# Optimization experiments

Measured on AMD Instinct MI355X. Metric: run time of the kernel, lower is better.

The kernel has to match this reference:

```python
import jax, jax.numpy as jnp
import numpy as np

NUM_HEADS = 16
NEG_INF = -1e9  # matches torch source's -1000000000.0 additive mask
ROPE_BASE = 10000.0


def _rope(t):
    """Rotary position embedding, half-rotation form. t: [B, H, S, D]."""
    D = t.shape[-1]
    S = t.shape[2]
    inv_freq = 1.0 / (ROPE_BASE ** (jnp.arange(0, D, 2, dtype=jnp.float32) / D))  # [D/2]
    pos = jnp.arange(S, dtype=jnp.float32)
    freqs = pos[:, None] * inv_freq[None, :]          # [S, D/2]
    cos = jnp.cos(freqs)[None, None]                  # [1,1,S,D/2]
    sin = jnp.sin(freqs)[None, None]
    t1, t2 = t[..., : D // 2], t[..., D // 2 :]
    return jnp.concatenate([t1 * cos - t2 * sin, t1 * sin + t2 * cos], axis=-1)


def setup_inputs() -> dict:
    key = jax.random.key(0)
    kx, kq, kk, kv, ko = jax.random.split(key, 5)
    B, S, Dm = 2, 2048, 1024
    w_scale = 0.02
    return {
        "x": jax.random.normal(kx, (B, S, Dm), dtype=jnp.float32),
        "attention_mask": jnp.ones((B, S), dtype=jnp.float32),
        "Wq": jax.random.normal(kq, (Dm, Dm), dtype=jnp.float32) * w_scale,
        "Wk": jax.random.normal(kk, (Dm, Dm), dtype=jnp.float32) * w_scale,
        "Wv": jax.random.normal(kv, (Dm, Dm), dtype=jnp.float32) * w_scale,
        "Wo": jax.random.normal(ko, (Dm, Dm), dtype=jnp.float32) * w_scale,
    }


def reference(x, attention_mask, Wq, Wk, Wv, Wo):
    B, S, Dm = x.shape
    H = NUM_HEADS
    Hd = Dm // H

    def to_heads(t):  # [B,S,Dm] -> [B,H,S,Hd]
        return t.reshape(B, S, H, Hd).transpose(0, 2, 1, 3)

    q = _rope(to_heads(x @ Wq))
    k = _rope(to_heads(x @ Wk))
    v = to_heads(x @ Wv)

    scaling = 1.0 / np.sqrt(Hd).astype(np.float32)
    scores = jnp.einsum("bhqd,bhkd->bhqk", q, k) * scaling  # [B,H,S,S]

    # causal additive mask (triu of -1e9 above diagonal), as in apply_masking
    causal = jnp.triu(jnp.full((S, S), NEG_INF, dtype=scores.dtype), k=1)
    # padding mask: (1 - mask) * -1e9 broadcast to [B,1,1,S]
    amask = (1.0 - attention_mask)[:, None, None, :] * NEG_INF
    scores = scores + causal[None, None] + amask

    weights = jax.nn.softmax(scores, axis=-1)
    out = jnp.einsum("bhqk,bhkd->bhqd", weights, v)  # [B,H,S,Hd]
    out = out.transpose(0, 2, 1, 3).reshape(B, S, Dm)
    return out @ Wo
```

## Files before the change

### kernel.cpp

```cpp
#include <hip/hip_runtime.h>

typedef unsigned short u16;
typedef unsigned int u32;
typedef __attribute__((ext_vector_type(8))) short short8;
typedef __attribute__((ext_vector_type(4))) short s4v;
typedef __attribute__((ext_vector_type(4))) float f32x4;

#define S_LEN 2048
#define NH 16
#define HD 64
#define DM 1024

#if __has_builtin(__builtin_amdgcn_mfma_f32_16x16x16_bf16)
#define MFMA_K16(a, b, c) __builtin_amdgcn_mfma_f32_16x16x16_bf16(a, b, c, 0, 0, 0)
#else
#define MFMA_K16(a, b, c) __builtin_amdgcn_mfma_f32_16x16x16bf16_1k(a, b, c, 0, 0, 0)
#endif

__device__ __forceinline__ u16 f2bf(float f) {
    union { float f; u32 u; } v; v.f = f;
    u32 u = v.u;
    u32 r = u + 0x7fffu + ((u >> 16) & 1u);
    return (u16)(r >> 16);
}
__device__ __forceinline__ float bf2f(u16 h) {
    union { u32 u; float f; } v; v.u = ((u32)h) << 16;
    return v.f;
}

__device__ __forceinline__ u32 cvtpk_bf16(float lo, float hi) {
    u32 r;
    asm("v_cvt_pk_bf16_f32 %0, %1, %2" : "=v"(r) : "v"(lo), "v"(hi));
    return r;
}

__device__ __forceinline__ void load_lds16(const u16* g, u16* l) {
    __builtin_amdgcn_global_load_lds((const __attribute__((address_space(1))) void*)g,
                                     (__attribute__((address_space(3))) void*)l, 16, 0, 0);
}

__global__ __launch_bounds__(256) void cvt_bf16(const float* __restrict__ in, u16* __restrict__ out, int n) {
    int i = (blockIdx.x * 256 + threadIdx.x) * 4;
    if (i < n) {
        float4 v = *(const float4*)(in + i);
        ushort4 o;
        o.x = f2bf(v.x); o.y = f2bf(v.y); o.z = f2bf(v.z); o.w = f2bf(v.w);
        *(ushort4*)(out + i) = o;
    }
}

__global__ __launch_bounds__(256) void transpose_w4(const float* __restrict__ W0, const float* __restrict__ W1,
                                                    const float* __restrict__ W2, const float* __restrict__ W3,
                                                    u16* __restrict__ T0, u16* __restrict__ T1,
                                                    u16* __restrict__ T2, u16* __restrict__ T3) {
    __shared__ float tile[32][33];
    int z = blockIdx.z;
    const float* W = (z == 0) ? W0 : (z == 1) ? W1 : (z == 2) ? W2 : W3;
    u16* Wt = (z == 0) ? T0 : (z == 1) ? T1 : (z == 2) ? T2 : T3;
    int tx = threadIdx.x, ty = threadIdx.y;
    int k0 = blockIdx.y * 32, n0 = blockIdx.x * 32;
    #pragma unroll
    for (int j = 0; j < 32; j += 8)
        tile[ty + j][tx] = W[(size_t)(k0 + ty + j) * DM + n0 + tx];
    __syncthreads();
    #pragma unroll
    for (int j = 0; j < 32; j += 8)
        Wt[(size_t)(n0 + ty + j) * DM + k0 + tx] = f2bf(tile[tx][ty + j]);
}

template<int MODE, int NI>
__global__ __launch_bounds__(256) void gemm128(const u16* __restrict__ A, const u16* __restrict__ Bt,
                                               u16* __restrict__ Qh, u16* __restrict__ Kh,
                                               u16* __restrict__ Vh, float* __restrict__ Cf) {
    __shared__ u16 Al[128 * 64];
    __shared__ u16 Bl[NI * 32 * 64];
    const int K = DM;
    int tid = threadIdx.x;
    int wave = tid >> 6, lane = tid & 63, g = lane >> 4, ln = lane & 15;
    int wm = (wave >> 1) * 64, wn = (wave & 1) * (NI * 16);
    size_t mb0 = (size_t)blockIdx.y * 128, nb0 = (size_t)blockIdx.x * (NI * 32);

    f32x4 acc[4][NI];
    #pragma unroll
    for (int i = 0; i < 4; i++)
        #pragma unroll
        for (int j = 0; j < NI; j++)
            acc[i][j] = (f32x4){0.f, 0.f, 0.f, 0.f};

    int srow = lane >> 3;
    int scol = (lane & 7) ^ srow;
    const u16* Ag = A + (mb0 + wave * 32 + srow) * K + scol * 8;
    u16* Alw = Al + wave * 2048;
    const u16* Bg;
    u16* Blw;
    if (NI == 4) {
        Bg = Bt + (nb0 + wave * 32 + srow) * K + scol * 8;
        Blw = Bl + wave * 2048;
    } else {
        Bg = Bt + (nb0 + wave * 16 + srow) * K + scol * 8;
        Blw = Bl + wave * 1024;
    }
    int cswz = ln & 7;

    for (int k0 = 0; k0 < K; k0 += 64) {
        __syncthreads();
        #pragma unroll
        for (int c = 0; c < 4; c++)
            load_lds16(Ag + (size_t)(c * 8) * K + k0, Alw + c * 512);
        #pragma unroll
        for (int c = 0; c < (NI == 4 ? 4 : 2); c++)
            load_lds16(Bg + (size_t)(c * 8) * K + k0, Blw + c * 512);
        __syncthreads();
        short8 af[2][4], bf[2][NI];
        #pragma unroll
        for (int ks = 0; ks < 2; ks++) {
            #pragma unroll
            for (int i = 0; i < 4; i++)
                af[ks][i] = *(const short8*)&Al[(wm + i * 16 + ln) * 64 + (((ks * 4 + g) ^ cswz) * 8)];
            #pragma unroll
            for (int i = 0; i < NI; i++)
                bf[ks][i] = *(const short8*)&Bl[(wn + i * 16 + ln) * 64 + (((ks * 4 + g) ^ cswz) * 8)];
        }
        #pragma unroll
        for (int ks = 0; ks < 2; ks++)
            #pragma unroll
            for (int mi = 0; mi < 4; mi++)
                #pragma unroll
                for (int ni = 0; ni < NI; ni++)
                    acc[mi][ni] = __builtin_amdgcn_mfma_f32_16x16x32_bf16(af[ks][mi], bf[ks][ni], acc[mi][ni], 0, 0, 0);
    }

    if (MODE == 1) {
        #pragma unroll
        for (int mi = 0; mi < 4; mi++)
            #pragma unroll
            for (int ni = 0; ni < NI; ni++)
                #pragma unroll
                for (int r = 0; r < 4; r++) {
                    int m = (int)mb0 + wm + mi * 16 + g * 4 + r;
                    int n = (int)nb0 + wn + ni * 16 + ln;
                    Cf[(size_t)m * DM + n] = acc[mi][ni][r];
                }
    } else {
        int nbase = (int)nb0 + wn;
        int which = nbase >> 10;
        int h = (nbase & (DM - 1)) >> 6;
        if (which < 2) {
            u16* dst = (which == 0) ? Qh : Kh;
            float inv0 = exp2f(-0.4152408746976557f * (float)ln);
            float inv1 = exp2f(-0.4152408746976557f * (float)(16 + ln));
            #pragma unroll
            for (int mi = 0; mi < 4; mi++) {
                #pragma unroll
                for (int r = 0; r < 4; r++) {
                    int m = (int)mb0 + wm + mi * 16 + g * 4 + r;
                    int b = m >> 11, s = m & (S_LEN - 1);
                    float fs = (float)s;
                    float sn0, cs0, sn1, cs1;
                    __sincosf(fs * inv0, &sn0, &cs0);
                    __sincosf(fs * inv1, &sn1, &cs1);
                    float a0 = acc[mi][0][r], a1 = acc[mi][1][r];
                    float a2 = acc[mi][2][r], a3 = acc[mi][3][r];
                    size_t base = ((size_t)(b * NH + h) * S_LEN + s) * HD;
                    dst[base + ln]      = f2bf(a0 * cs0 - a2 * sn0);
                    dst[base + 16 + ln] = f2bf(a1 * cs1 - a3 * sn1);
                    dst[base + 32 + ln] = f2bf(a0 * sn0 + a2 * cs0);
                    dst[base + 48 + ln] = f2bf(a1 * sn1 + a3 * cs1);
                }
            }
        } else {
            #pragma unroll
            for (int mi = 0; mi < 4; mi++) {
                #pragma unroll
                for (int r = 0; r < 4; r++) {
                    int m = (int)mb0 + wm + mi * 16 + g * 4 + r;
                    int b = m >> 11, s = m & (S_LEN - 1);
                    size_t base = ((size_t)(b * NH + h) * S_LEN + s) * HD;
                    #pragma unroll
                    for (int ni = 0; ni < 4; ni++)
                        Vh[base + ni * 16 + ln] = f2bf(acc[mi][ni][r]);
                }
            }
        }
    }
}

__global__ __launch_bounds__(256) void vtrans(const u16* __restrict__ Vh, u16* __restrict__ Vt) {
    __shared__ u16 t[64][70];
    int tid = threadIdx.x;
    int s0 = blockIdx.x * 64, bh = blockIdx.y;
    int r = tid >> 2, c = (tid & 3) * 8;
    const u16* src = Vh + ((size_t)bh * S_LEN + s0) * HD;
    *(short8*)&t[r][c]      = *(const short8*)(src + (size_t)r * HD + c);
    *(short8*)&t[r][c + 32] = *(const short8*)(src + (size_t)r * HD + c + 32);
    __syncthreads();
    u16* dst = Vt + ((size_t)bh * HD + r) * S_LEN + s0;
    short8 o0, o1;
    #pragma unroll
    for (int j = 0; j < 8; j++) {
        o0[j] = (short)t[c + j][r];
        o1[j] = (short)t[c + 32 + j][r];
    }
    *(short8*)(dst + c)      = o0;
    *(short8*)(dst + c + 32) = o1;
}

__global__ __launch_bounds__(512, 4) void flash_kernel(const u16* __restrict__ Qh, const u16* __restrict__ Kh,
                                                       const u16* __restrict__ Vt, const float* __restrict__ amask,
                                                       u16* __restrict__ Op0, u16* __restrict__ Op1,
                                                       u16* __restrict__ Op2, u16* __restrict__ Op3,
                                                       float* __restrict__ L0, float* __restrict__ L1,
                                                       float* __restrict__ L2, float* __restrict__ L3) {
    __shared__ u16 Kl[2][64 * 64];
    __shared__ u16 Vl[2][64 * 64];
    __shared__ float Ml[2][64];
    int tid = threadIdx.x;
    int wave = tid >> 6, lane = tid & 63, g = lane >> 4, ln = lane & 15;
    int qblk = 15 - ((int)blockIdx.x >> 2);
    int sp = blockIdx.x & 3;
    int bh = blockIdx.y;
    int b = bh >> 4;
    int q0 = qblk * 128 + wave * 16;
    int qv = q0 + ln;
    const u16* Qb = Qh + (size_t)bh * (S_LEN * HD);
    const u16* Kb = Kh + (size_t)bh * (S_LEN * HD);
    const u16* Vb = Vt + (size_t)bh * (S_LEN * HD);
    const float* am = amask + b * S_LEN;

    short8 qa0 = *(const short8*)(Qb + (size_t)(q0 + ln) * HD + g * 8);
    short8 qa1 = *(const short8*)(Qb + (size_t)(q0 + ln) * HD + 32 + g * 8);

    f32x4 O[4];
    #pragma unroll
    for (int i = 0; i < 4; i++) O[i] = (f32x4){0.f, 0.f, 0.f, 0.f};
    float lsum = 0.f;
    const float SCL = 0.125f * 1.4426950408889634f;
    const float MSCL = -1.4426950408889634e9f;

    int T = 2 * qblk + 2;
    int srow = tid >> 3, scid = tid & 7, s7 = srow & 7;
    int stoff = srow * 64 + ((scid ^ s7) * 8);
    const u16* KgL = Kb + (size_t)srow * HD + ((scid ^ s7) * 8);
    const u16* VgP = Vb + (size_t)srow * S_LEN + scid * 8;
    bool vswap = (wave & 1);

    int l7 = ln & 7;
    int kc0 = (g ^ l7) * 8;
    int kc1 = ((4 + g) ^ l7) * 8;
    int rbq = ln * 64;
    int vcoff[4];
    #pragma unroll
    for (int n0 = 0; n0 < 4; n0++)
        vcoff[n0] = (((n0 * 2 + (g >> 1)) ^ l7) * 8) + ((((g & 1) ^ (ln >> 3)) & 1) * 4);

    load_lds16(KgL + (size_t)(sp * 64) * HD, &Kl[0][wave * 512]);
    short8 vR = *(const short8*)(VgP + sp * 64);
    float mR = 0.f;
    if (tid < 64) mR = (1.0f - am[sp * 64 + tid]) * MSCL;
    int cur = 0;

    for (int kt = sp; kt < T; kt += 4) {
        int kbase = kt * 64;
        short8 vS = vR;
        if (vswap) vS = __builtin_shufflevector(vR, vR, 4, 5, 6, 7, 0, 1, 2, 3);
        *(short8*)(Vl[cur] + stoff) = vS;
        if (tid < 64) Ml[cur][tid] = mR;
        __syncthreads();

        if (kt + 4 < T) {
            load_lds16(KgL + (size_t)(kbase + 256) * HD, &Kl[cur ^ 1][wave * 512]);
            vR = *(const short8*)(VgP + (kbase + 256));
            if (tid < 64) mR = (1.0f - am[kbase + 256 + tid]) * MSCL;
        }

        if (kbase <= q0 + 15) {
            const u16* Klc = Kl[cur];
            const u16* Vlc = Vl[cur];
            u32 pk[4][2];
            bool needmask = (kbase + 63 > q0);

            if (!needmask) {
                #pragma unroll
                for (int n0 = 0; n0 < 4; n0++) {
                    const u16* kr = Klc + (n0 * 16) * 64 + rbq;
                    short8 kb0 = *(const short8*)(kr + kc0);
                    short8 kb1 = *(const short8*)(kr + kc1);
                    f32x4 sv = (f32x4){0.f, 0.f, 0.f, 0.f};
                    sv = __builtin_amdgcn_mfma_f32_16x16x32_bf16(kb0, qa0, sv, 0, 0, 0);
                    sv = __builtin_amdgcn_mfma_f32_16x16x32_bf16(kb1, qa1, sv, 0, 0, 0);
                    f32x4 mkv = *(f32x4*)&Ml[cur][n0 * 16 + g * 4];
                    float p[4];
                    #pragma unroll
                    for (int r = 0; r < 4; r++) {
                        p[r] = exp2f(sv[r] * SCL + mkv[r]);
                        lsum += p[r];
                    }
                    pk[n0][0] = cvtpk_bf16(p[0], p[1]);
                    pk[n0][1] = cvtpk_bf16(p[2], p[3]);
                }
            } else {
                #pragma unroll
                for (int n0 = 0; n0 < 4; n0++) {
                    const u16* kr = Klc + (n0 * 16) * 64 + rbq;
                    short8 kb0 = *(const short8*)(kr + kc0);
                    short8 kb1 = *(const short8*)(kr + kc1);
                    f32x4 sv = (f32x4){0.f, 0.f, 0.f, 0.f};
                    sv = __builtin_amdgcn_mfma_f32_16x16x32_bf16(kb0, qa0, sv, 0, 0, 0);
                    sv = __builtin_amdgcn_mfma_f32_16x16x32_bf16(kb1, qa1, sv, 0, 0, 0);
                    f32x4 mkv = *(f32x4*)&Ml[cur][n0 * 16 + g * 4];
                    int keyb = kbase + n0 * 16 + g * 4;
                    float p[4];
                    #pragma unroll
                    for (int r = 0; r < 4; r++) {
                        float s2 = sv[r] * SCL + mkv[r];
                        if (keyb + r > qv) s2 = -1.0e9f;
                        p[r] = exp2f(s2);
                        lsum += p[r];
                    }
                    pk[n0][0] = cvtpk_bf16(p[0], p[1]);
                    pk[n0][1] = cvtpk_bf16(p[2], p[3]);
                }
            }

            __builtin_amdgcn_s_setprio(1);
            #pragma unroll
            for (int t = 0; t < 4; t++) {
                const u16* vr = Vlc + (t * 16) * 64 + rbq;
                #pragma unroll
                for (int n0 = 0; n0 < 4; n0++) {
                    s4v va = *(const s4v*)(vr + vcoff[n0]);
                    union { u32 u[2]; s4v v; } pb;
                    pb.u[0] = pk[n0][0];
                    pb.u[1] = pk[n0][1];
                    O[t] = MFMA_K16(va, pb.v, O[t]);
                }
            }
            __builtin_amdgcn_s_setprio(0);
        }
        cur ^= 1;
    }

    lsum += __shfl_xor(lsum, 16, 64);
    lsum += __shfl_xor(lsum, 32, 64);
    u16* Od = (sp == 0) ? Op0 : (sp == 1) ? Op1 : (sp == 2) ? Op2 : Op3;
    float* Ld = (sp == 0) ? L0 : (sp == 1) ? L1 : (sp == 2) ? L2 : L3;
    if (lane < 16) Ld[(size_t)bh * S_LEN + q0 + ln] = lsum;
    size_t obase = (size_t)bh * (HD * S_LEN) + q0 + ln;
    #pragma unroll
    for (int t = 0; t < 4; t++)
        #pragma unroll
        for (int r = 0; r < 4; r++)
            Od[obase + (size_t)(t * 16 + g * 4 + r) * S_LEN] = f2bf(O[t][r]);
}

__global__ __launch_bounds__(256) void flash_reduce(const u16* __restrict__ Op0, const u16* __restrict__ Op1,
                                                    const u16* __restrict__ Op2, const u16* __restrict__ Op3,
                                                    const float* __restrict__ L0, const float* __restrict__ L1,
                                                    const float* __restrict__ L2, const float* __restrict__ L3,
                                                    u16* __restrict__ attn) {
    __shared__ float t[64][65];
    int tid = threadIdx.x;
    int qt = blockIdx.x, bh = blockIdx.y;
    int b = bh >> 4, h = bh & (NH - 1);
    #pragma unroll
    for (int it = 0; it < 2; it++) {
        int idx = tid + it * 256;
        int d = idx >> 3, c = (idx & 7) * 8;
        size_t off = (size_t)bh * (HD * S_LEN) + (size_t)d * S_LEN + qt * 64 + c;
        short8 a0 = *(const short8*)(Op0 + off);
        short8 a1 = *(const short8*)(Op1 + off);
        short8 a2 = *(const short8*)(Op2 + off);
        short8 a3 = *(const short8*)(Op3 + off);
        #pragma unroll
        for (int j = 0; j < 8; j++)
            t[d][c + j] = bf2f((u16)a0[j]) + bf2f((u16)a1[j]) + bf2f((u16)a2[j]) + bf2f((u16)a3[j]);
    }
    __syncthreads();
    int qr = tid >> 2, dc = (tid & 3) * 16;
    int qg = qt * 64 + qr;
    size_t li = (size_t)bh * S_LEN + qg;
    float inv = 1.0f / (L0[li] + L1[li] + L2[li] + L3[li]);
    short8 o0, o1;
    #pragma unroll
    for (int j = 0; j < 8; j++) {
        o0[j] = (short)f2bf(t[dc + j][qr] * inv);
        o1[j] = (short)f2bf(t[dc + 8 + j][qr] * inv);
    }
    u16* dst = attn + ((size_t)b * S_LEN + qg) * DM + h * HD + dc;
    *(short8*)dst = o0;
    *(short8*)(dst + 8) = o1;
}

extern "C" void kernel_launch(void* const* d_in, const int* in_sizes, int n_in,
                              void* d_out, int out_size, void* d_ws, size_t ws_size,
                              hipStream_t stream) {
    const float* x     = (const float*)d_in[0];
    const float* amask = (const float*)d_in[1];
    const float* Wq    = (const float*)d_in[2];
    const float* Wk    = (const float*)d_in[3];
    const float* Wv    = (const float*)d_in[4];
    const float* Wo    = (const float*)d_in[5];
    float* out = (float*)d_out;
    char* ws = (char*)d_ws;

    u16* x_bf   = (u16*)(ws);
    u16* Op1    = (u16*)(ws);
    u16* Wqkv_t = (u16*)(ws + 8388608);
    float* L0   = (float*)(ws + 8388608);
    float* L1   = (float*)(ws + 8650752);
    float* L2   = (float*)(ws + 8912896);
    float* L3   = (float*)(ws + 9175040);
    u16* Wo_t   = (u16*)(ws + 14680064);
    u16* Qh     = (u16*)(ws + 16777216);
    u16* Kh     = (u16*)(ws + 25165824);
    u16* Vt     = (u16*)(ws + 33554432);
    u16* attnF  = (u16*)(ws + 33554432);
    u16* Vh     = (u16*)(ws + 41943040);
    u16* Op0    = (u16*)(ws + 41943040);
    u16* Op2    = (u16*)d_out;
    u16* Op3    = (u16*)d_out + 4194304;

    cvt_bf16<<<4096, 256, 0, stream>>>(x, x_bf, 2 * S_LEN * DM);

    transpose_w4<<<dim3(32, 32, 4), dim3(32, 8), 0, stream>>>(
        Wq, Wk, Wv, Wo, Wqkv_t, Wqkv_t + 1048576, Wqkv_t + 2097152, Wo_t);

    gemm128<0, 4><<<dim3(24, 32), 256, 0, stream>>>(x_bf, Wqkv_t, Qh, Kh, Vh, nullptr);

    vtrans<<<dim3(32, 2 * NH), 256, 0, stream>>>(Vh, Vt);

    flash_kernel<<<dim3(64, 2 * NH), 512, 0, stream>>>(Qh, Kh, Vt, amask,
                                                       Op0, Op1, Op2, Op3, L0, L1, L2, L3);

    flash_reduce<<<dim3(32, 2 * NH), 256, 0, stream>>>(Op0, Op1, Op2, Op3,
                                                       L0, L1, L2, L3, attnF);

    gemm128<1, 2><<<dim3(16, 32), 256, 0, stream>>>(attnF, Wo_t, nullptr, nullptr, nullptr, out);
}
```

Baseline: 208.2 us.

## Load V tiles via direct-to-LDS async copy and precompute mask into registers

The vtrans kernel now writes V pre-swizzled, with the half-swap applied for odd row groups, and precomputes the scaled additive padding mask into a workspace buffer. The flash kernel then streams V tiles into LDS with the same direct global-to-LDS path used for K, and loads the mask straight into registers, removing the register-staged V store and the shared mask array. It also splits the row-sum accumulator into four independent lanes to shorten the dependency chain. This relies on the swizzle in vtrans matching the read offsets in flash and on the new workspace region not overlapping live buffers.

```diff
diff --git a/kernel.cpp b/kernel.cpp
--- a/kernel.cpp
+++ b/kernel.cpp
@@ -10,6 +10,7 @@
 #define NH 16
 #define HD 64
 #define DM 1024
+#define MSCL_C (-1.4426950408889634e9f)
 
 #if __has_builtin(__builtin_amdgcn_mfma_f32_16x16x16_bf16)
 #define MFMA_K16(a, b, c) __builtin_amdgcn_mfma_f32_16x16x16_bf16(a, b, c, 0, 0, 0)
@@ -185,10 +186,15 @@
     }
 }
 
-__global__ __launch_bounds__(256) void vtrans(const u16* __restrict__ Vh, u16* __restrict__ Vt) {
+__global__ __launch_bounds__(256) void vtrans(const u16* __restrict__ Vh, u16* __restrict__ Vt,
+                                              const float* __restrict__ amask, float* __restrict__ Mg) {
     __shared__ u16 t[64][70];
     int tid = threadIdx.x;
     int s0 = blockIdx.x * 64, bh = blockIdx.y;
+    if (bh == 0) {
+        int idx = blockIdx.x * 256 + tid;
+        if (idx < 2 * S_LEN) Mg[idx] = (1.0f - amask[idx]) * MSCL_C;
+    }
     int r = tid >> 2, c = (tid & 3) * 8;
     const u16* src = Vh + ((size_t)bh * S_LEN + s0) * HD;
     *(short8*)&t[r][c]      = *(const short8*)(src + (size_t)r * HD + c);
@@ -201,19 +207,22 @@
         o0[j] = (short)t[c + j][r];
         o1[j] = (short)t[c + 32 + j][r];
     }
+    if (r & 8) {
+        o0 = __builtin_shufflevector(o0, o0, 4, 5, 6, 7, 0, 1, 2, 3);
+        o1 = __builtin_shufflevector(o1, o1, 4, 5, 6, 7, 0, 1, 2, 3);
+    }
     *(short8*)(dst + c)      = o0;
     *(short8*)(dst + c + 32) = o1;
 }
 
 __global__ __launch_bounds__(512, 4) void flash_kernel(const u16* __restrict__ Qh, const u16* __restrict__ Kh,
-                                                       const u16* __restrict__ Vt, const float* __restrict__ amask,
+                                                       const u16* __restrict__ Vt, const float* __restrict__ Mg,
                                                        u16* __restrict__ Op0, u16* __restrict__ Op1,
                                                        u16* __restrict__ Op2, u16* __restrict__ Op3,
                                                        float* __restrict__ L0, float* __restrict__ L1,
                                                        float* __restrict__ L2, float* __restrict__ L3) {
     __shared__ u16 Kl[2][64 * 64];
     __shared__ u16 Vl[2][64 * 64];
-    __shared__ float Ml[2][64];
     int tid = threadIdx.x;
     int wave = tid >> 6, lane = tid & 63, g = lane >> 4, ln = lane & 15;
     int qblk = 15 - ((int)blockIdx.x >> 2);
@@ -225,7 +234,7 @@
     const u16* Qb = Qh + (size_t)bh * (S_LEN * HD);
     const u16* Kb = Kh + (size_t)bh * (S_LEN * HD);
     const u16* Vb = Vt + (size_t)bh * (S_LEN * HD);
-    const float* am = amask + b * S_LEN;
+    const float* Mb = Mg + b * S_LEN;
 
     short8 qa0 = *(const short8*)(Qb + (size_t)(q0 + ln) * HD + g * 8);
     short8 qa1 = *(const short8*)(Qb + (size_t)(q0 + ln) * HD + 32 + g * 8);
@@ -233,16 +242,13 @@
     f32x4 O[4];
     #pragma unroll
     for (int i = 0; i < 4; i++) O[i] = (f32x4){0.f, 0.f, 0.f, 0.f};
-    float lsum = 0.f;
+    f32x4 ls = (f32x4){0.f, 0.f, 0.f, 0.f};
     const float SCL = 0.125f * 1.4426950408889634f;
-    const float MSCL = -1.4426950408889634e9f;
 
     int T = 2 * qblk + 2;
     int srow = tid >> 3, scid = tid & 7, s7 = srow & 7;
-    int stoff = srow * 64 + ((scid ^ s7) * 8);
     const u16* KgL = Kb + (size_t)srow * HD + ((scid ^ s7) * 8);
-    const u16* VgP = Vb + (size_t)srow * S_LEN + scid * 8;
-    bool vswap = (wave & 1);
+    const u16* VgL = Vb + (size_t)srow * S_LEN + ((scid ^ s7) * 8);
 
     int l7 = ln & 7;
     int kc0 = (g ^ l7) * 8;
@@ -254,23 +260,27 @@
         vcoff[n0] = (((n0 * 2 + (g >> 1)) ^ l7) * 8) + ((((g & 1) ^ (ln >> 3)) & 1) * 4);
 
     load_lds16(KgL + (size_t)(sp * 64) * HD, &Kl[0][wave * 512]);
-    short8 vR = *(const short8*)(VgP + sp * 64);
-    float mR = 0.f;
-    if (tid < 64) mR = (1.0f - am[sp * 64 + tid]) * MSCL;
+    load_lds16(VgL + sp * 64, &Vl[0][wave * 512]);
+    f32x4 mkR[4];
+    #pragma unroll
+    for (int n0 = 0; n0 < 4; n0++)
+        mkR[n0] = *(const f32x4*)(Mb + sp * 64 + n0 * 16 + g * 4);
     int cur = 0;
 
     for (int kt = sp; kt < T; kt += 4) {
         int kbase = kt * 64;
-        short8 vS = vR;
-        if (vswap) vS = __builtin_shufflevector(vR, vR, 4, 5, 6, 7, 0, 1, 2, 3);
-        *(short8*)(Vl[cur] + stoff) = vS;
-        if (tid < 64) Ml[cur][tid] = mR;
         __syncthreads();
+
+        f32x4 mk[4];
+        #pragma unroll
+        for (int n0 = 0; n0 < 4; n0++) mk[n0] = mkR[n0];
 
         if (kt + 4 < T) {
             load_lds16(KgL + (size_t)(kbase + 256) * HD, &Kl[cur ^ 1][wave * 512]);
-            vR = *(const short8*)(VgP + (kbase + 256));
-            if (tid < 64) mR = (1.0f - am[kbase + 256 + tid]) * MSCL;
+            load_lds16(VgL + (kbase + 256), &Vl[cur ^ 1][wave * 512]);
+            #pragma unroll
+            for (int n0 = 0; n0 < 4; n0++)
+                mkR[n0] = *(const f32x4*)(Mb + kbase + 256 + n0 * 16 + g * 4);
         }
 
         if (kbase <= q0 + 15) {
@@ -288,12 +298,11 @@
                     f32x4 sv = (f32x4){0.f, 0.f, 0.f, 0.f};
                     sv = __builtin_amdgcn_mfma_f32_16x16x32_bf16(kb0, qa0, sv, 0, 0, 0);
                     sv = __builtin_amdgcn_mfma_f32_16x16x32_bf16(kb1, qa1, sv, 0, 0, 0);
-                    f32x4 mkv = *(f32x4*)&Ml[cur][n0 * 16 + g * 4];
                     float p[4];
                     #pragma unroll
                     for (int r = 0; r < 4; r++) {
-                        p[r] = exp2f(sv[r] * SCL + mkv[r]);
-                        lsum += p[r];
+                        p[r] = exp2f(sv[r] * SCL + mk[n0][r]);
+                        ls[r] += p[r];
                     }
                     pk[n0][0] = cvtpk_bf16(p[0], p[1]);
                     pk[n0][1] = cvtpk_bf16(p[2], p[3]);
@@ -307,15 +316,14 @@
                     f32x4 sv = (f32x4){0.f, 0.f, 0.f, 0.f};
                     sv = __builtin_amdgcn_mfma_f32_16x16x32_bf16(kb0, qa0, sv, 0, 0, 0);
                     sv = __builtin_amdgcn_mfma_f32_16x16x32_bf16(kb1, qa1, sv, 0, 0, 0);
-                    f32x4 mkv = *(f32x4*)&Ml[cur][n0 * 16 + g * 4];
                     int keyb = kbase + n0 * 16 + g * 4;
                     float p[4];
                     #pragma unroll
                     for (int r = 0; r < 4; r++) {
-                        float s2 = sv[r] * SCL + mkv[r];
+                        float s2 = sv[r] * SCL + mk[n0][r];
                         if (keyb + r > qv) s2 = -1.0e9f;
                         p[r] = exp2f(s2);
-                        lsum += p[r];
+                        ls[r] += p[r];
                     }
                     pk[n0][0] = cvtpk_bf16(p[0], p[1]);
                     pk[n0][1] = cvtpk_bf16(p[2], p[3]);
@@ -340,6 +348,7 @@
         cur ^= 1;
     }
 
+    float lsum = (ls[0] + ls[1]) + (ls[2] + ls[3]);
     lsum += __shfl_xor(lsum, 16, 64);
     lsum += __shfl_xor(lsum, 32, 64);
     u16* Od = (sp == 0) ? Op0 : (sp == 1) ? Op1 : (sp == 2) ? Op2 : Op3;
@@ -410,6 +419,7 @@
     float* L1   = (float*)(ws + 8650752);
     float* L2   = (float*)(ws + 8912896);
     float* L3   = (float*)(ws + 9175040);
+    float* Mg   = (float*)(ws + 9437184);
     u16* Wo_t   = (u16*)(ws + 14680064);
     u16* Qh     = (u16*)(ws + 16777216);
     u16* Kh     = (u16*)(ws + 25165824);
@@ -427,9 +437,9 @@
 
     gemm128<0, 4><<<dim3(24, 32), 256, 0, stream>>>(x_bf, Wqkv_t, Qh, Kh, Vh, nullptr);
 
-    vtrans<<<dim3(32, 2 * NH), 256, 0, stream>>>(Vh, Vt);
-
-    flash_kernel<<<dim3(64, 2 * NH), 512, 0, stream>>>(Qh, Kh, Vt, amask,
+    vtrans<<<dim3(32, 2 * NH), 256, 0, stream>>>(Vh, Vt, amask, Mg);
+
+    flash_kernel<<<dim3(64, 2 * NH), 512, 0, stream>>>(Qh, Kh, Vt, Mg,
                                                        Op0, Op1, Op2, Op3, L0, L1, L2, L3);
 
     flash_reduce<<<dim3(32, 2 * NH), 256, 0, stream>>>(Op0, Op1, Op2, Op3,
```

Result: slower. 214.3 us (+2.9%).
